# Kernel tuning notes

Hardware: AMD Instinct MI355X
Metric: run time of the kernel (lower is better)

The kernel has to match this reference:

```python
import jax, jax.numpy as jnp
import numpy as np
import math

B, N, Q, K = 1, 64, 512, 512
C_Q = C_K = C_V = 256
C_HIDDEN = 32
NO_HEADS = 8
HID = C_HIDDEN * NO_HEADS  # 256


def setup_inputs() -> dict:
    key = jax.random.key(0)
    ks = jax.random.split(key, 12)
    inp = {
        "q_x": jax.random.normal(ks[0], (B, N, Q, C_Q), jnp.float32),
        "k_x": jax.random.normal(ks[1], (B, N, K, C_K), jnp.float32),
        "v_x": jax.random.normal(ks[2], (B, N, K, C_V), jnp.float32),
        "bias_mask": jax.random.normal(ks[3], (B, N, 1, 1, K), jnp.float32),
        "bias_pair": jax.random.normal(ks[4], (B, 1, NO_HEADS, Q, K), jnp.float32),
        # projection weights stored [in, out] (torch Linear is [out, in])
        "wq": jax.random.normal(ks[5], (C_Q, HID), jnp.float32) / math.sqrt(C_Q),
        "wk": jax.random.normal(ks[6], (C_K, HID), jnp.float32) / math.sqrt(C_K),
        "wv": jax.random.normal(ks[7], (C_V, HID), jnp.float32) / math.sqrt(C_V),
        # gating: init weights=0, bias=1 in the module; use small random for a non-trivial test
        "wg": jax.random.normal(ks[8], (C_Q, HID), jnp.float32) * 0.02,
        "bg": jnp.ones((HID,), jnp.float32),
        # output: init 'final' (zeros); use small random for a non-trivial test
        "wo": jax.random.normal(ks[9], (HID, C_Q), jnp.float32) * 0.02,
        "bo": jnp.zeros((C_Q,), jnp.float32),
    }
    return inp


def reference(q_x, k_x, v_x, bias_mask, bias_pair, wq, wk, wv, wg, bg, wo, bo):
    h, c = NO_HEADS, C_HIDDEN
    # projections -> [B, N, Q/K, H, C_h]
    q = (q_x @ wq).reshape(*q_x.shape[:-1], h, c) / math.sqrt(c)
    k = (k_x @ wk).reshape(*k_x.shape[:-1], h, c)
    v = (v_x @ wv).reshape(*v_x.shape[:-1], h, c)
    # logits [B, N, H, Q, K] with additive biases
    a = jnp.einsum("bnqhc,bnkhc->bnhqk", q, k) + bias_mask + bias_pair
    a = jax.nn.softmax(a, axis=-1)
    # output [B, N, Q, H, C_h]
    o = jnp.einsum("bnhqk,bnkhc->bnqhc", a, v)
    # gating
    g = jax.nn.sigmoid((q_x @ wg + bg).reshape(*q_x.shape[:-1], h, c))
    o = o * g
    o = o.reshape(*o.shape[:-2], h * c)
    return o @ wo + bo
```

## Files before the change

kernel.cpp:

```cpp
#include <hip/hip_runtime.h>
#include <math.h>

#define NSEQ   64
#define QLEN   512
#define KLEN   512
#define CIN    256
#define HEADS  8
#define CH     32
#define HIDDIM 256
#define M_TOTAL (NSEQ * QLEN)

typedef _Float16 f16x8 __attribute__((ext_vector_type(8)));
typedef _Float16 f16x4 __attribute__((ext_vector_type(4)));
typedef __fp16   fp16x2 __attribute__((ext_vector_type(2)));
typedef float    f32x4 __attribute__((ext_vector_type(4)));

__device__ __forceinline__ void gload16(const void* g, void* l) {
    __builtin_amdgcn_global_load_lds(
        (const __attribute__((address_space(1))) void*)g,
        (__attribute__((address_space(3))) void*)l, 16, 0, 0);
}

__global__ __launch_bounds__(256) void wcast_kernel(
    const float* __restrict__ w0, const float* __restrict__ w1,
    const float* __restrict__ w2, const float* __restrict__ w3,
    const float* __restrict__ w4, _Float16* __restrict__ wt)
{
    __shared__ float t[64][65];
    const float* W;
    switch (blockIdx.z) {
        case 0: W = w0; break; case 1: W = w1; break;
        case 2: W = w2; break; case 3: W = w3; break;
        default: W = w4;
    }
    _Float16* WT = wt + (size_t)blockIdx.z * 65536;
    const int i0 = blockIdx.x * 64, o0 = blockIdx.y * 64;
    const int tid = threadIdx.x;
    const int rr = tid >> 4, c4 = tid & 15;
    #pragma unroll
    for (int i = 0; i < 4; ++i) {
        const int row = rr + i * 16;
        *(float4*)&t[row][c4 * 4] = *(const float4*)&W[(size_t)(i0 + row) * 256 + o0 + c4 * 4];
    }
    __syncthreads();
    #pragma unroll
    for (int i = 0; i < 4; ++i) {
        const int row = rr + i * 16;
        f16x4 v;
        #pragma unroll
        for (int j = 0; j < 4; ++j) v[j] = (_Float16)t[c4 * 4 + j][row];
        *(f16x4*)&WT[(size_t)(o0 + row) * 256 + i0 + c4 * 4] = v;
    }
}

__global__ __launch_bounds__(256) void bpfrag_kernel(
    const float* __restrict__ bias_pair, float* __restrict__ frag)
{
    __shared__ float t[64][68];
    const int qb = blockIdx.x, kb = blockIdx.y, h = blockIdx.z;
    const int tid = threadIdx.x;
    #pragma unroll
    for (int i = 0; i < 4; ++i) {
        const int idx = tid + i * 256;
        const int r = idx >> 4, c4 = idx & 15;
        *(float4*)&t[r][c4 * 4] = *(const float4*)
            &bias_pair[((size_t)h * QLEN + qb * 64 + r) * KLEN + kb * 64 + c4 * 4];
    }
    __syncthreads();
    const int lane = tid & 63, w = tid >> 6;
    const int l15 = lane & 15, quad = lane >> 4;
    const int qt = qb * 4 + w;
    #pragma unroll
    for (int kt2 = 0; kt2 < 4; ++kt2) {
        const int kt = kb * 4 + kt2;
        float4 v;
        v.x = t[w * 16 + l15][kt2 * 16 + quad * 4 + 0];
        v.y = t[w * 16 + l15][kt2 * 16 + quad * 4 + 1];
        v.z = t[w * 16 + l15][kt2 * 16 + quad * 4 + 2];
        v.w = t[w * 16 + l15][kt2 * 16 + quad * 4 + 3];
        *(float4*)&frag[(((size_t)(h * 32 + qt) * 32) + kt) * 256 + lane * 4] = v;
    }
}

__global__ __launch_bounds__(256, 2) void proj_gemm_kernel(
    const float* __restrict__ q_x, const float* __restrict__ k_x,
    const float* __restrict__ v_x, const _Float16* __restrict__ wT,
    const float* __restrict__ bg,
    _Float16* __restrict__ oq, _Float16* __restrict__ ok,
    _Float16* __restrict__ ovT, _Float16* __restrict__ og)
{
    __shared__ __attribute__((aligned(16))) float A_s[2][32 * 256];

    const int combo = blockIdx.x >> 6;
    const int blk   = blockIdx.x & 63;
    const int mode  = combo >> 1;
    const int nhalf = combo & 1;
    const float* A = (mode <= 1) ? q_x : (mode == 2) ? k_x : v_x;
    const _Float16* BT = wT + (size_t)mode * 65536;

    const int tid  = threadIdx.x;
    const int lane = tid & 63, w = tid >> 6;
    const int l15  = lane & 15, quad = lane >> 4;
    const int nw   = nhalf * 128 + w * 32;

    f16x8 bfr[2][8];
    #pragma unroll
    for (int nt = 0; nt < 2; ++nt)
        #pragma unroll
        for (int ks = 0; ks < 8; ++ks)
            bfr[nt][ks] = *(const f16x8*)(BT +
                (size_t)(nw + nt * 16 + l15) * 256 + ks * 32 + quad * 8);

    float bgv[2] = {0.f, 0.f};
    if (mode == 1) { bgv[0] = bg[nw + l15]; bgv[1] = bg[nw + 16 + l15]; }

    const int row_base = blk * 512;

    f32x4 acc[2][2];
    #pragma unroll
    for (int mt = 0; mt < 2; ++mt)
        #pragma unroll
        for (int nt = 0; nt < 2; ++nt) acc[mt][nt] = (f32x4){0.f, 0.f, 0.f, 0.f};

    auto stage = [&](int panel, int buf) {
        const int row0 = row_base + panel * 32;
        #pragma unroll
        for (int j = 0; j < 8; ++j) {
            const int p = tid + j * 256;
            const int r = p >> 6, c = p & 63;
            const int cl = (c & ~7) | ((c & 7) ^ (r & 7));
            gload16(A + (size_t)(row0 + r) * 256 + cl * 4, &A_s[buf][p * 4]);
        }
    };

    stage(0, 0);
    __syncthreads();

    for (int i = 0; i < 16; ++i) {
        if (i < 15) stage(i + 1, (i + 1) & 1);
        const int buf = i & 1;

        #pragma unroll
        for (int ks = 0; ks < 8; ++ks) {
            f16x8 af[2];
            #pragma unroll
            for (int mt = 0; mt < 2; ++mt) {
                const int r  = mt * 16 + l15;
                const int x0 = ks * 8 + ((quad * 2 + 0) ^ (r & 7));
                const int x1 = ks * 8 + ((quad * 2 + 1) ^ (r & 7));
                const f32x4 a0 = *(const f32x4*)&A_s[buf][(r * 64 + x0) * 4];
                const f32x4 a1 = *(const f32x4*)&A_s[buf][(r * 64 + x1) * 4];
                f16x8 v;
                v[0] = (_Float16)a0[0]; v[1] = (_Float16)a0[1];
                v[2] = (_Float16)a0[2]; v[3] = (_Float16)a0[3];
                v[4] = (_Float16)a1[0]; v[5] = (_Float16)a1[1];
                v[6] = (_Float16)a1[2]; v[7] = (_Float16)a1[3];
                af[mt] = v;
            }
            #pragma unroll
            for (int mt = 0; mt < 2; ++mt)
                #pragma unroll
                for (int nt = 0; nt < 2; ++nt)
                    acc[mt][nt] = __builtin_amdgcn_mfma_f32_16x16x32_f16(
                        af[mt], bfr[nt][ks], acc[mt][nt], 0, 0, 0);
        }

        const int row0 = row_base + i * 32;
        if (mode == 3) {
            #pragma unroll
            for (int mt = 0; mt < 2; ++mt) {
                #pragma unroll
                for (int nt = 0; nt < 2; ++nt) {
                    const int col  = nw + nt * 16 + l15;
                    const int rowg = row0 + mt * 16 + quad * 4;
                    const int nn = rowg >> 9, kpos = rowg & 511;
                    f16x4 st;
                    #pragma unroll
                    for (int reg = 0; reg < 4; ++reg) st[reg] = (_Float16)acc[mt][nt][reg];
                    *(f16x4*)&ovT[((size_t)(nn * 256 + col)) * 512 + kpos] = st;
                }
            }
        } else {
            _Float16* C = (mode == 0) ? oq : (mode == 1) ? og : ok;
            #pragma unroll
            for (int mt = 0; mt < 2; ++mt) {
                #pragma unroll
                for (int nt = 0; nt < 2; ++nt) {
                    const int col  = nw + nt * 16 + l15;
                    const int rowg = row0 + mt * 16 + quad * 4;
                    #pragma unroll
                    for (int reg = 0; reg < 4; ++reg) {
                        float x = acc[mt][nt][reg];
                        if (mode == 0) x *= 0.17677669529663689f;
                        if (mode == 1) { x += bgv[nt]; x = 1.0f / (1.0f + __expf(-x)); }
                        C[(size_t)(rowg + reg) * HIDDIM + col] = (_Float16)x;
                    }
                }
            }
        }
        #pragma unroll
        for (int mt = 0; mt < 2; ++mt)
            #pragma unroll
            for (int nt = 0; nt < 2; ++nt) acc[mt][nt] = (f32x4){0.f, 0.f, 0.f, 0.f};

        __syncthreads();
    }
}

__global__ __launch_bounds__(256, 2) void gemm_mfma_kernel(
    const _Float16* __restrict__ Ain, const _Float16* __restrict__ BT,
    const float* __restrict__ bias, float* __restrict__ Cout)
{
    __shared__ __attribute__((aligned(16))) _Float16 A_s[2][128 * 64];
    __shared__ __attribute__((aligned(16))) _Float16 B_s[2][128 * 64];
    const int m0 = blockIdx.x * 128, n0 = blockIdx.y * 128;
    const int tid = threadIdx.x;
    const int lane = tid & 63, w = tid >> 6;
    const int l15 = lane & 15, quad = lane >> 4;
    const int mw = (w & 1) * 64, nw = (w >> 1) * 64;

    f32x4 acc[4][4];
    #pragma unroll
    for (int mt = 0; mt < 4; ++mt)
        #pragma unroll
        for (int nt = 0; nt < 4; ++nt) acc[mt][nt] = (f32x4){0.f, 0.f, 0.f, 0.f};

    #pragma unroll
    for (int j = 0; j < 4; ++j) {
        const int p = tid + j * 256;
        const int r = p >> 3;
        const int lc = (p & 7) ^ (r & 7);
        gload16(Ain + (size_t)(m0 + r) * CIN + lc * 8, &A_s[0][p * 8]);
        gload16(BT  + (size_t)(n0 + r) * CIN + lc * 8, &B_s[0][p * 8]);
    }
    __syncthreads();

    int buf = 0;
    for (int kk = 0; kk < 4; ++kk) {
        if (kk < 3) {
            const int k0n = (kk + 1) * 64;
            #pragma unroll
            for (int j = 0; j < 4; ++j) {
                const int p = tid + j * 256;
                const int r = p >> 3;
                const int lc = (p & 7) ^ (r & 7);
                gload16(Ain + (size_t)(m0 + r) * CIN + k0n + lc * 8, &A_s[buf ^ 1][p * 8]);
                gload16(BT  + (size_t)(n0 + r) * CIN + k0n + lc * 8, &B_s[buf ^ 1][p * 8]);
            }
        }
        #pragma unroll
        for (int ks = 0; ks < 2; ++ks) {
            f16x8 af[4], bf[4];
            #pragma unroll
            for (int mt = 0; mt < 4; ++mt) {
                const int arow = mw + mt * 16 + l15;
                const int ac = (ks * 4 + quad) ^ (arow & 7);
                af[mt] = *(const f16x8*)&A_s[buf][arow * 64 + ac * 8];
            }
            #pragma unroll
            for (int nt = 0; nt < 4; ++nt) {
                const int brow = nw + nt * 16 + l15;
                const int bc = (ks * 4 + quad) ^ (brow & 7);
                bf[nt] = *(const f16x8*)&B_s[buf][brow * 64 + bc * 8];
            }
            #pragma unroll
            for (int mt = 0; mt < 4; ++mt)
                #pragma unroll
                for (int nt = 0; nt < 4; ++nt)
                    acc[mt][nt] = __builtin_amdgcn_mfma_f32_16x16x32_f16(
                        af[mt], bf[nt], acc[mt][nt], 0, 0, 0);
        }
        if (kk < 3) { __syncthreads(); buf ^= 1; }
    }

    #pragma unroll
    for (int mt = 0; mt < 4; ++mt) {
        #pragma unroll
        for (int nt = 0; nt < 4; ++nt) {
            const int col = n0 + nw + nt * 16 + l15;
            const int rowb = m0 + mw + mt * 16 + quad * 4;
            #pragma unroll
            for (int reg = 0; reg < 4; ++reg) {
                const float x = acc[mt][nt][reg] + bias[col];
                Cout[(size_t)(rowb + reg) * HIDDIM + col] = x;
            }
        }
    }
}

__global__ __launch_bounds__(256, 4) void attn_kernel(
    const _Float16* __restrict__ qb, const _Float16* __restrict__ kb,
    const _Float16* __restrict__ vT, const _Float16* __restrict__ gb,
    _Float16* __restrict__ ob,
    const float* __restrict__ bias_mask, const float* __restrict__ bp_frag)
{
    __shared__ _Float16 k_s[128][40];
    __shared__ _Float16 v_s[32][136];

    const int n    = blockIdx.x;
    const int h    = blockIdx.y;
    const int q0   = blockIdx.z * 128;
    const int tid  = threadIdx.x;
    const int lane = tid & 63;
    const int wq   = tid >> 6;
    const int l15  = lane & 15;
    const int quad = lane >> 4;

    f16x8 qf[2];
    #pragma unroll
    for (int qt = 0; qt < 2; ++qt)
        qf[qt] = *(const f16x8*)(qb +
            (size_t)(n * QLEN + q0 + wq * 32 + qt * 16 + l15) * HIDDIM + h * CH + quad * 8);

    const float* bpf = bp_frag +
        ((size_t)(h * 32 + blockIdx.z * 8 + wq * 2) * 32) * 256 + lane * 4;
    const float* bmb = bias_mask + n * KLEN + quad * 4;

    f32x4 o_acc[2][2];
    float l_lane[2] = {0.f, 0.f};
    #pragma unroll
    for (int qt = 0; qt < 2; ++qt)
        #pragma unroll
        for (int ct = 0; ct < 2; ++ct) o_acc[qt][ct] = (f32x4){0.f, 0.f, 0.f, 0.f};

    const f32x4 z4 = (f32x4){0.f, 0.f, 0.f, 0.f};

    for (int ch = 0; ch < 4; ++ch) {
        __syncthreads();
        #pragma unroll
        for (int i = 0; i < 2; ++i) {
            const int idx = tid + i * 256;
            const int r = idx >> 2, c8 = idx & 3;
            *(uint4*)&k_s[r][c8 * 8] = *(const uint4*)
                (kb + (size_t)(n * KLEN + ch * 128 + r) * HIDDIM + h * CH + c8 * 8);
            const int vr = idx >> 4, vs = idx & 15;
            *(uint4*)&v_s[vr][vs * 8] = *(const uint4*)
                (vT + ((size_t)(n * HEADS + h) * CH + vr) * KLEN + ch * 128 + vs * 8);
        }
        __syncthreads();

        #pragma unroll
        for (int kt = 0; kt < 8; ++kt) {
            const int kti = ch * 8 + kt;
            const f16x8 kf = *(const f16x8*)&k_s[kt * 16 + l15][quad * 8];
            const f32x4 s0 = __builtin_amdgcn_mfma_f32_16x16x32_f16(kf, qf[0], z4, 0, 0, 0);
            const f32x4 s1 = __builtin_amdgcn_mfma_f32_16x16x32_f16(kf, qf[1], z4, 0, 0, 0);
            const float4 bm = *(const float4*)(bmb + ch * 128 + kt * 16);
            const f16x4 bv0 = *(const f16x4*)&v_s[l15][kt * 16 + quad * 4];
            const f16x4 bv1 = *(const f16x4*)&v_s[16 + l15][kt * 16 + quad * 4];
            #pragma unroll
            for (int qt = 0; qt < 2; ++qt) {
                const f32x4 s = qt ? s1 : s0;
                const float4 bp = *(const float4*)(bpf + ((size_t)qt * 32 + kti) * 256);
                const float p0 = __expf(s[0] + bm.x + bp.x - 4.0f);
                const float p1 = __expf(s[1] + bm.y + bp.y - 4.0f);
                const float p2 = __expf(s[2] + bm.z + bp.z - 4.0f);
                const float p3 = __expf(s[3] + bm.w + bp.w - 4.0f);
                l_lane[qt] += (p0 + p1) + (p2 + p3);
                union { f16x4 v; fp16x2 h[2]; } u;
                u.h[0] = __builtin_amdgcn_cvt_pkrtz(p0, p1);
                u.h[1] = __builtin_amdgcn_cvt_pkrtz(p2, p3);
                o_acc[qt][0] = __builtin_amdgcn_mfma_f32_16x16x16f16(u.v, bv0, o_acc[qt][0], 0, 0, 0);
                o_acc[qt][1] = __builtin_amdgcn_mfma_f32_16x16x16f16(u.v, bv1, o_acc[qt][1], 0, 0, 0);
            }
        }
    }

    float invl[2][4];
    #pragma unroll
    for (int qt = 0; qt < 2; ++qt) {
        float lf = l_lane[qt];
        lf += __shfl_xor(lf, 16);
        lf += __shfl_xor(lf, 32);
        #pragma unroll
        for (int reg = 0; reg < 4; ++reg)
            invl[qt][reg] = 1.0f / __shfl(lf, quad * 4 + reg);
    }

    #pragma unroll
    for (int qt = 0; qt < 2; ++qt) {
        #pragma unroll
        for (int ct = 0; ct < 2; ++ct) {
            #pragma unroll
            for (int reg = 0; reg < 4; ++reg) {
                const int row = q0 + wq * 32 + qt * 16 + quad * 4 + reg;
                const size_t idx = (size_t)(n * QLEN + row) * HIDDIM + h * CH + ct * 16 + l15;
                const float g = (float)gb[idx];
                ob[idx] = (_Float16)(o_acc[qt][ct][reg] * invl[qt][reg] * g);
            }
        }
    }
}

extern "C" void kernel_launch(void* const* d_in, const int* in_sizes, int n_in,
                              void* d_out, int out_size, void* d_ws, size_t ws_size,
                              hipStream_t stream)
{
    const float* q_x       = (const float*)d_in[0];
    const float* k_x       = (const float*)d_in[1];
    const float* v_x       = (const float*)d_in[2];
    const float* bias_mask = (const float*)d_in[3];
    const float* bias_pair = (const float*)d_in[4];
    const float* wq        = (const float*)d_in[5];
    const float* wk        = (const float*)d_in[6];
    const float* wv        = (const float*)d_in[7];
    const float* wg        = (const float*)d_in[8];
    const float* bg        = (const float*)d_in[9];
    const float* wo        = (const float*)d_in[10];
    const float* bo        = (const float*)d_in[11];
    float* out = (float*)d_out;

    const size_t BUF = (size_t)M_TOTAL * HIDDIM;
    _Float16* ws_q  = (_Float16*)d_ws;
    _Float16* ws_k  = ws_q + BUF;
    _Float16* ws_vT = ws_k + BUF;
    _Float16* ws_g  = ws_vT + BUF;
    _Float16* ws_o  = ws_g + BUF;
    _Float16* wT    = ws_o + BUF;
    float*    bpf   = (float*)(wT + 5 * 65536);

    wcast_kernel<<<dim3(4, 4, 5), 256, 0, stream>>>(wq, wg, wk, wv, wo, wT);
    bpfrag_kernel<<<dim3(8, 8, 8), 256, 0, stream>>>(bias_pair, bpf);

    proj_gemm_kernel<<<dim3(512), 256, 0, stream>>>(
        q_x, k_x, v_x, wT, bg, ws_q, ws_k, ws_vT, ws_g);

    attn_kernel<<<dim3(NSEQ, HEADS, QLEN / 128), 256, 0, stream>>>(
        ws_q, ws_k, ws_vT, ws_g, ws_o, bias_mask, bpf);

    gemm_mfma_kernel<<<dim3(M_TOTAL / 128, 2), 256, 0, stream>>>(
        ws_o, wT + 4 * 65536, bo, out);
}
```

Measured before the change: 263.7 us.

## Fold log2e and biases into MFMA accumulator, use exp2, restructure output projection

Pre-scales the q projection, the pair bias and the mask bias by log2(e), with the softmax offset folded into the pair-bias fragments. The attention loop then seeds the QK MFMA accumulator with the combined bias and calls a raw exp2, removing the per-element adds and the exp scaling. It also prefetches the next bias values one step ahead and raises wave priority around the MFMAs. Separately, the output projection is rewritten to hold the weight fragments in registers and stream 32-row A panels, replacing the 128x128 LDS-tiled GEMM. This adds an extra small kernel and workspace for the scaled mask.

```diff
diff --git a/kernel.cpp b/kernel.cpp
--- a/kernel.cpp
+++ b/kernel.cpp
@@ -9,6 +9,7 @@
 #define CH     32
 #define HIDDIM 256
 #define M_TOTAL (NSEQ * QLEN)
+#define L2E    1.4426950408889634f
 
 typedef _Float16 f16x8 __attribute__((ext_vector_type(8)));
 typedef _Float16 f16x4 __attribute__((ext_vector_type(4)));
@@ -19,6 +20,14 @@
     __builtin_amdgcn_global_load_lds(
         (const __attribute__((address_space(1))) void*)g,
         (__attribute__((address_space(3))) void*)l, 16, 0, 0);
+}
+
+__device__ __forceinline__ float exp2_fast(float x) {
+#if __has_builtin(__builtin_amdgcn_exp2f)
+    return __builtin_amdgcn_exp2f(x);
+#else
+    float r; asm("v_exp_f32 %0, %1" : "=v"(r) : "v"(x)); return r;
+#endif
 }
 
 __global__ __launch_bounds__(256) void wcast_kernel(
@@ -74,12 +83,21 @@
     for (int kt2 = 0; kt2 < 4; ++kt2) {
         const int kt = kb * 4 + kt2;
         float4 v;
-        v.x = t[w * 16 + l15][kt2 * 16 + quad * 4 + 0];
-        v.y = t[w * 16 + l15][kt2 * 16 + quad * 4 + 1];
-        v.z = t[w * 16 + l15][kt2 * 16 + quad * 4 + 2];
-        v.w = t[w * 16 + l15][kt2 * 16 + quad * 4 + 3];
+        v.x = (t[w * 16 + l15][kt2 * 16 + quad * 4 + 0] - 4.0f) * L2E;
+        v.y = (t[w * 16 + l15][kt2 * 16 + quad * 4 + 1] - 4.0f) * L2E;
+        v.z = (t[w * 16 + l15][kt2 * 16 + quad * 4 + 2] - 4.0f) * L2E;
+        v.w = (t[w * 16 + l15][kt2 * 16 + quad * 4 + 3] - 4.0f) * L2E;
         *(float4*)&frag[(((size_t)(h * 32 + qt) * 32) + kt) * 256 + lane * 4] = v;
     }
+}
+
+__global__ __launch_bounds__(256) void bmscale_kernel(
+    const float* __restrict__ bm, float* __restrict__ o)
+{
+    const int i = blockIdx.x * 256 + threadIdx.x;
+    float4 v = *(const float4*)(bm + (size_t)i * 4);
+    v.x *= L2E; v.y *= L2E; v.z *= L2E; v.w *= L2E;
+    *(float4*)(o + (size_t)i * 4) = v;
 }
 
 __global__ __launch_bounds__(256, 2) void proj_gemm_kernel(
@@ -191,7 +209,7 @@
                     #pragma unroll
                     for (int reg = 0; reg < 4; ++reg) {
                         float x = acc[mt][nt][reg];
-                        if (mode == 0) x *= 0.17677669529663689f;
+                        if (mode == 0) x *= 0.2550348614f;
                         if (mode == 1) { x += bgv[nt]; x = 1.0f / (1.0f + __expf(-x)); }
                         C[(size_t)(rowg + reg) * HIDDIM + col] = (_Float16)x;
                     }
@@ -207,84 +225,89 @@
     }
 }
 
-__global__ __launch_bounds__(256, 2) void gemm_mfma_kernel(
+__global__ __launch_bounds__(256, 2) void outproj_kernel(
     const _Float16* __restrict__ Ain, const _Float16* __restrict__ BT,
     const float* __restrict__ bias, float* __restrict__ Cout)
 {
-    __shared__ __attribute__((aligned(16))) _Float16 A_s[2][128 * 64];
-    __shared__ __attribute__((aligned(16))) _Float16 B_s[2][128 * 64];
-    const int m0 = blockIdx.x * 128, n0 = blockIdx.y * 128;
-    const int tid = threadIdx.x;
+    __shared__ __attribute__((aligned(16))) _Float16 A_s[2][32 * 256];
+
+    const int blk   = blockIdx.x & 255;
+    const int nhalf = blockIdx.x >> 8;
+    const int tid  = threadIdx.x;
     const int lane = tid & 63, w = tid >> 6;
-    const int l15 = lane & 15, quad = lane >> 4;
-    const int mw = (w & 1) * 64, nw = (w >> 1) * 64;
-
-    f32x4 acc[4][4];
-    #pragma unroll
-    for (int mt = 0; mt < 4; ++mt)
-        #pragma unroll
-        for (int nt = 0; nt < 4; ++nt) acc[mt][nt] = (f32x4){0.f, 0.f, 0.f, 0.f};
-
-    #pragma unroll
-    for (int j = 0; j < 4; ++j) {
-        const int p = tid + j * 256;
-        const int r = p >> 3;
-        const int lc = (p & 7) ^ (r & 7);
-        gload16(Ain + (size_t)(m0 + r) * CIN + lc * 8, &A_s[0][p * 8]);
-        gload16(BT  + (size_t)(n0 + r) * CIN + lc * 8, &B_s[0][p * 8]);
-    }
+    const int l15  = lane & 15, quad = lane >> 4;
+    const int nw   = nhalf * 128 + w * 32;
+
+    f16x8 bfr[2][8];
+    #pragma unroll
+    for (int nt = 0; nt < 2; ++nt)
+        #pragma unroll
+        for (int ks = 0; ks < 8; ++ks)
+            bfr[nt][ks] = *(const f16x8*)(BT +
+                (size_t)(nw + nt * 16 + l15) * 256 + ks * 32 + quad * 8);
+
+    const float bv[2] = { bias[nw + l15], bias[nw + 16 + l15] };
+    const int row_base = blk * 128;
+
+    f32x4 acc[2][2];
+    #pragma unroll
+    for (int mt = 0; mt < 2; ++mt)
+        #pragma unroll
+        for (int nt = 0; nt < 2; ++nt) acc[mt][nt] = (f32x4){0.f, 0.f, 0.f, 0.f};
+
+    auto stage = [&](int panel, int buf) {
+        const int row0 = row_base + panel * 32;
+        #pragma unroll
+        for (int j = 0; j < 4; ++j) {
+            const int p = tid + j * 256;
+            const int r = p >> 5, c = p & 31;
+            const int cl = (c & ~7) | ((c & 7) ^ (r & 7));
+            gload16(Ain + (size_t)(row0 + r) * 256 + cl * 8, &A_s[buf][p * 8]);
+        }
+    };
+
+    stage(0, 0);
     __syncthreads();
 
-    int buf = 0;
-    for (int kk = 0; kk < 4; ++kk) {
-        if (kk < 3) {
-            const int k0n = (kk + 1) * 64;
-            #pragma unroll
-            for (int j = 0; j < 4; ++j) {
-                const int p = tid + j * 256;
-                const int r = p >> 3;
-                const int lc = (p & 7) ^ (r & 7);
-                gload16(Ain + (size_t)(m0 + r) * CIN + k0n + lc * 8, &A_s[buf ^ 1][p * 8]);
-                gload16(BT  + (size_t)(n0 + r) * CIN + k0n + lc * 8, &B_s[buf ^ 1][p * 8]);
-            }
-        }
-        #pragma unroll
-        for (int ks = 0; ks < 2; ++ks) {
-            f16x8 af[4], bf[4];
-            #pragma unroll
-            for (int mt = 0; mt < 4; ++mt) {
-                const int arow = mw + mt * 16 + l15;
-                const int ac = (ks * 4 + quad) ^ (arow & 7);
-                af[mt] = *(const f16x8*)&A_s[buf][arow * 64 + ac * 8];
-            }
-            #pragma unroll
-            for (int nt = 0; nt < 4; ++nt) {
-                const int brow = nw + nt * 16 + l15;
-                const int bc = (ks * 4 + quad) ^ (brow & 7);
-                bf[nt] = *(const f16x8*)&B_s[buf][brow * 64 + bc * 8];
-            }
-            #pragma unroll
-            for (int mt = 0; mt < 4; ++mt)
+    for (int i = 0; i < 4; ++i) {
+        if (i < 3) stage(i + 1, (i + 1) & 1);
+        const int buf = i & 1;
+
+        #pragma unroll
+        for (int ks = 0; ks < 8; ++ks) {
+            f16x8 af[2];
+            #pragma unroll
+            for (int mt = 0; mt < 2; ++mt) {
+                const int r = mt * 16 + l15;
+                const int c = (ks * 4 + quad) ^ (r & 7);
+                af[mt] = *(const f16x8*)&A_s[buf][r * 256 + c * 8];
+            }
+            #pragma unroll
+            for (int mt = 0; mt < 2; ++mt)
                 #pragma unroll
-                for (int nt = 0; nt < 4; ++nt)
+                for (int nt = 0; nt < 2; ++nt)
                     acc[mt][nt] = __builtin_amdgcn_mfma_f32_16x16x32_f16(
-                        af[mt], bf[nt], acc[mt][nt], 0, 0, 0);
-        }
-        if (kk < 3) { __syncthreads(); buf ^= 1; }
-    }
-
-    #pragma unroll
-    for (int mt = 0; mt < 4; ++mt) {
-        #pragma unroll
-        for (int nt = 0; nt < 4; ++nt) {
-            const int col = n0 + nw + nt * 16 + l15;
-            const int rowb = m0 + mw + mt * 16 + quad * 4;
-            #pragma unroll
-            for (int reg = 0; reg < 4; ++reg) {
-                const float x = acc[mt][nt][reg] + bias[col];
-                Cout[(size_t)(rowb + reg) * HIDDIM + col] = x;
-            }
-        }
+                        af[mt], bfr[nt][ks], acc[mt][nt], 0, 0, 0);
+        }
+
+        const int row0 = row_base + i * 32;
+        #pragma unroll
+        for (int mt = 0; mt < 2; ++mt) {
+            #pragma unroll
+            for (int nt = 0; nt < 2; ++nt) {
+                const int col  = nw + nt * 16 + l15;
+                const int rowg = row0 + mt * 16 + quad * 4;
+                #pragma unroll
+                for (int reg = 0; reg < 4; ++reg)
+                    Cout[(size_t)(rowg + reg) * HIDDIM + col] = acc[mt][nt][reg] + bv[nt];
+            }
+        }
+        #pragma unroll
+        for (int mt = 0; mt < 2; ++mt)
+            #pragma unroll
+            for (int nt = 0; nt < 2; ++nt) acc[mt][nt] = (f32x4){0.f, 0.f, 0.f, 0.f};
+
+        __syncthreads();
     }
 }
 
@@ -292,7 +315,7 @@
     const _Float16* __restrict__ qb, const _Float16* __restrict__ kb,
     const _Float16* __restrict__ vT, const _Float16* __restrict__ gb,
     _Float16* __restrict__ ob,
-    const float* __restrict__ bias_mask, const float* __restrict__ bp_frag)
+    const float* __restrict__ bm2, const float* __restrict__ bp_frag)
 {
     __shared__ _Float16 k_s[128][40];
     __shared__ _Float16 v_s[32][136];
@@ -314,7 +337,7 @@
 
     const float* bpf = bp_frag +
         ((size_t)(h * 32 + blockIdx.z * 8 + wq * 2) * 32) * 256 + lane * 4;
-    const float* bmb = bias_mask + n * KLEN + quad * 4;
+    const float* bmb = bm2 + n * KLEN + quad * 4;
 
     f32x4 o_acc[2][2];
     float l_lane[2] = {0.f, 0.f};
@@ -323,7 +346,9 @@
         #pragma unroll
         for (int ct = 0; ct < 2; ++ct) o_acc[qt][ct] = (f32x4){0.f, 0.f, 0.f, 0.f};
 
-    const f32x4 z4 = (f32x4){0.f, 0.f, 0.f, 0.f};
+    float4 bmv = *(const float4*)bmb;
+    float4 bp0 = *(const float4*)bpf;
+    float4 bp1 = *(const float4*)(bpf + 32 * 256);
 
     for (int ch = 0; ch < 4; ++ch) {
         __syncthreads();
@@ -343,25 +368,37 @@
         for (int kt = 0; kt < 8; ++kt) {
             const int kti = ch * 8 + kt;
             const f16x8 kf = *(const f16x8*)&k_s[kt * 16 + l15][quad * 8];
-            const f32x4 s0 = __builtin_amdgcn_mfma_f32_16x16x32_f16(kf, qf[0], z4, 0, 0, 0);
-            const f32x4 s1 = __builtin_amdgcn_mfma_f32_16x16x32_f16(kf, qf[1], z4, 0, 0, 0);
-            const float4 bm = *(const float4*)(bmb + ch * 128 + kt * 16);
+            f32x4 c0, c1;
+            c0[0] = bmv.x + bp0.x; c0[1] = bmv.y + bp0.y;
+            c0[2] = bmv.z + bp0.z; c0[3] = bmv.w + bp0.w;
+            c1[0] = bmv.x + bp1.x; c1[1] = bmv.y + bp1.y;
+            c1[2] = bmv.z + bp1.z; c1[3] = bmv.w + bp1.w;
+            __builtin_amdgcn_s_setprio(1);
+            const f32x4 s0 = __builtin_amdgcn_mfma_f32_16x16x32_f16(kf, qf[0], c0, 0, 0, 0);
+            const f32x4 s1 = __builtin_amdgcn_mfma_f32_16x16x32_f16(kf, qf[1], c1, 0, 0, 0);
+            __builtin_amdgcn_s_setprio(0);
+            if (kti < 31) {
+                bmv = *(const float4*)(bmb + (size_t)(kti + 1) * 16);
+                bp0 = *(const float4*)(bpf + (size_t)(kti + 1) * 256);
+                bp1 = *(const float4*)(bpf + (size_t)(32 + kti + 1) * 256);
+            }
             const f16x4 bv0 = *(const f16x4*)&v_s[l15][kt * 16 + quad * 4];
             const f16x4 bv1 = *(const f16x4*)&v_s[16 + l15][kt * 16 + quad * 4];
             #pragma unroll
             for (int qt = 0; qt < 2; ++qt) {
                 const f32x4 s = qt ? s1 : s0;
-                const float4 bp = *(const float4*)(bpf + ((size_t)qt * 32 + kti) * 256);
-                const float p0 = __expf(s[0] + bm.x + bp.x - 4.0f);
-                const float p1 = __expf(s[1] + bm.y + bp.y - 4.0f);
-                const float p2 = __expf(s[2] + bm.z + bp.z - 4.0f);
-                const float p3 = __expf(s[3] + bm.w + bp.w - 4.0f);
+                const float p0 = exp2_fast(s[0]);
+                const float p1 = exp2_fast(s[1]);
+                const float p2 = exp2_fast(s[2]);
+                const float p3 = exp2_fast(s[3]);
                 l_lane[qt] += (p0 + p1) + (p2 + p3);
                 union { f16x4 v; fp16x2 h[2]; } u;
                 u.h[0] = __builtin_amdgcn_cvt_pkrtz(p0, p1);
                 u.h[1] = __builtin_amdgcn_cvt_pkrtz(p2, p3);
+                __builtin_amdgcn_s_setprio(1);
                 o_acc[qt][0] = __builtin_amdgcn_mfma_f32_16x16x16f16(u.v, bv0, o_acc[qt][0], 0, 0, 0);
                 o_acc[qt][1] = __builtin_amdgcn_mfma_f32_16x16x16f16(u.v, bv1, o_acc[qt][1], 0, 0, 0);
+                __builtin_amdgcn_s_setprio(0);
             }
         }
     }
@@ -418,16 +455,18 @@
     _Float16* ws_o  = ws_g + BUF;
     _Float16* wT    = ws_o + BUF;
     float*    bpf   = (float*)(wT + 5 * 65536);
+    float*    bm2   = bpf + (size_t)8 * 512 * 512;
 
     wcast_kernel<<<dim3(4, 4, 5), 256, 0, stream>>>(wq, wg, wk, wv, wo, wT);
     bpfrag_kernel<<<dim3(8, 8, 8), 256, 0, stream>>>(bias_pair, bpf);
+    bmscale_kernel<<<dim3(32), 256, 0, stream>>>(bias_mask, bm2);
 
     proj_gemm_kernel<<<dim3(512), 256, 0, stream>>>(
         q_x, k_x, v_x, wT, bg, ws_q, ws_k, ws_vT, ws_g);
 
     attn_kernel<<<dim3(NSEQ, HEADS, QLEN / 128), 256, 0, stream>>>(
-        ws_q, ws_k, ws_vT, ws_g, ws_o, bias_mask, bpf);
-
-    gemm_mfma_kernel<<<dim3(M_TOTAL / 128, 2), 256, 0, stream>>>(
+        ws_q, ws_k, ws_vT, ws_g, ws_o, bm2, bpf);
+
+    outproj_kernel<<<dim3(512), 256, 0, stream>>>(
         ws_o, wT + 4 * 65536, bo, out);
 }
```

Result: slower. 407.8 us (+54.7%).
